# Kernel tuning notes

Hardware: AMD Instinct MI355X
Metric: run time of the kernel (lower is better)

## Reference

```python
import jax, jax.numpy as jnp
import numpy as np

B, S, H = 2, 2048, 1024
E, I = 8, 4096
TOP_K = 2
W_SCALE = 0.02


def setup_inputs() -> dict:
    key = jax.random.key(0)
    k1, k2, k3, k4, k5 = jax.random.split(key, 5)
    return {
        "hidden_states": jax.random.normal(k1, (B, S, H), dtype=jnp.float32),
        "gate_w": jax.random.normal(k2, (H, E), dtype=jnp.float32) * W_SCALE,
        "w1s": jax.random.normal(k3, (E, H, I), dtype=jnp.float32) * W_SCALE,
        "w2s": jax.random.normal(k4, (E, I, H), dtype=jnp.float32) * W_SCALE,
        "w3s": jax.random.normal(k5, (E, H, I), dtype=jnp.float32) * W_SCALE,
    }


def reference(hidden_states, gate_w, w1s, w2s, w3s):
    b, s, h = hidden_states.shape
    x = hidden_states.reshape(-1, h)                      # [T, H]
    # Router: softmax in fp32, top-k, renormalize (matches torch F.softmax(dtype=float) + topk)
    logits = x @ gate_w                                   # [T, E]
    probs = jax.nn.softmax(logits.astype(jnp.float32), axis=-1)
    rw, sel = jax.lax.top_k(probs, TOP_K)                 # [T, K], [T, K]
    rw = rw / jnp.sum(rw, axis=-1, keepdims=True)
    # Per-token combine weight for each expert: [T, E]
    comb = jnp.sum(jax.nn.one_hot(sel, E, dtype=x.dtype) * rw[..., None].astype(x.dtype), axis=1)
    # Expert SwiGLU MLPs; loop over small fixed expert count (same math as grouped GEMM + scatter)
    out = jnp.zeros_like(x)
    for e in range(E):
        inter = jax.nn.silu(x @ w1s[e]) * (x @ w3s[e])    # [T, I]
        out = out + comb[:, e:e + 1] * (inter @ w2s[e])   # [T, H]
    return out.reshape(b, s, h)
```

## Files before the change

kernel.cpp:

```cpp
#include <hip/hip_runtime.h>

#define T_TOK 4096
#define H_DIM 1024
#define I_DIM 4096
#define NE 8
#define INTER_ROWS 9216

typedef _Float16 f16;
typedef _Float16 f16x8 __attribute__((ext_vector_type(8)));
typedef _Float16 f16x4 __attribute__((ext_vector_type(4)));
typedef float f32x4 __attribute__((ext_vector_type(4)));

#define GLOBAL_AS __attribute__((address_space(1)))
#define LDS_AS __attribute__((address_space(3)))

__device__ __forceinline__ void gload_lds16(const void* g, void* l) {
  __builtin_amdgcn_global_load_lds((GLOBAL_AS const unsigned int*)g,
                                   (LDS_AS unsigned int*)l, 16, 0, 0);
}

__global__ void cast_x_kernel(const float* __restrict__ x, f16* __restrict__ xh) {
  int i = blockIdx.x * 256 + threadIdx.x;
  float4 v = reinterpret_cast<const float4*>(x)[i];
  f16x4 o = {(f16)v.x, (f16)v.y, (f16)v.z, (f16)v.w};
  reinterpret_cast<f16x4*>(xh)[i] = o;
}

__global__ __launch_bounds__(256) void transpose_cast_kernel(
    const float* __restrict__ w, f16* __restrict__ wt, int R, int C) {
  __shared__ float tile[64][65];
  const int z = blockIdx.z;
  const float* in = w + (size_t)z * R * C;
  f16* out = wt + (size_t)z * R * C;
  const int c0 = blockIdx.x * 64, r0 = blockIdx.y * 64;
  const int tr = threadIdx.x >> 4;
  const int tc = (threadIdx.x & 15) * 4;
#pragma unroll
  for (int i = 0; i < 4; ++i) {
    int r = tr + i * 16;
    float4 v = *reinterpret_cast<const float4*>(&in[(size_t)(r0 + r) * C + c0 + tc]);
    tile[r][tc] = v.x; tile[r][tc + 1] = v.y; tile[r][tc + 2] = v.z; tile[r][tc + 3] = v.w;
  }
  __syncthreads();
#pragma unroll
  for (int i = 0; i < 4; ++i) {
    int oc = tr + i * 16;
    f16x4 h;
#pragma unroll
    for (int j = 0; j < 4; ++j) h[j] = (f16)tile[tc + j][oc];
    *reinterpret_cast<f16x4*>(&out[(size_t)(c0 + oc) * R + r0 + tc]) = h;
  }
}

__global__ void router_kernel(const float* __restrict__ x, const float* __restrict__ gw,
                              int* __restrict__ counts, int* __restrict__ lists,
                              float* __restrict__ wgts) {
  const int t = blockIdx.x;
  const int l = threadIdx.x;
  const float* xr = x + (size_t)t * H_DIM;
  float acc[NE];
#pragma unroll
  for (int e = 0; e < NE; ++e) acc[e] = 0.f;
  for (int k = l; k < H_DIM; k += 64) {
    float xv = xr[k];
#pragma unroll
    for (int e = 0; e < NE; ++e) acc[e] += xv * gw[k * NE + e];
  }
#pragma unroll
  for (int e = 0; e < NE; ++e) {
    float v = acc[e];
#pragma unroll
    for (int off = 32; off > 0; off >>= 1) v += __shfl_xor(v, off);
    acc[e] = v;
  }
  if (l == 0) {
    int i1 = 0;
#pragma unroll
    for (int e = 1; e < NE; ++e)
      if (acc[e] > acc[i1]) i1 = e;
    int i2 = (i1 == 0) ? 1 : 0;
#pragma unroll
    for (int e = 0; e < NE; ++e)
      if (e != i1 && acc[e] > acc[i2]) i2 = e;
    float wA = 1.f / (1.f + __expf(acc[i2] - acc[i1]));
    float wB = 1.f - wA;
    int p1 = atomicAdd(&counts[i1], 1);
    lists[i1 * T_TOK + p1] = t;
    wgts[i1 * T_TOK + p1] = wA;
    int p2 = atomicAdd(&counts[i2], 1);
    lists[i2 * T_TOK + p2] = t;
    wgts[i2 * T_TOK + p2] = wB;
  }
}

__global__ void prefix_kernel(const int* __restrict__ counts, int* __restrict__ bases) {
  if (threadIdx.x == 0) {
    int s = 0;
#pragma unroll
    for (int e = 0; e < NE; ++e) {
      bases[e] = s;
      s += (counts[e] + 127) & ~127;
    }
  }
}

__global__ __launch_bounds__(256, 2) void gemm_a_kernel(
    const f16* __restrict__ xh, const f16* __restrict__ w1t, const f16* __restrict__ w3t,
    const int* __restrict__ counts, const int* __restrict__ bases,
    const int* __restrict__ lists, f16* __restrict__ inter) {
  const int z = blockIdx.z;
  const int cnt = counts[z];
  const int r0 = blockIdx.y * 128;
  if (r0 >= cnt) return;
  const int base = bases[z];
  const int c0 = blockIdx.x * 128;
  const int tid = threadIdx.x;
  const int lane = tid & 63;
  const int wid = tid >> 6;
  const int wm = wid >> 1, wn = wid & 1;
  const int lrow = lane & 15, lk = lane >> 4;

  __shared__ __align__(16) f16 As[128 * 64];
  __shared__ __align__(16) f16 B1s[128 * 64];
  __shared__ __align__(16) f16 B3s[128 * 64];

  const int* lst = lists + z * T_TOK;
  const f16* w1 = w1t + (size_t)z * H_DIM * I_DIM;
  const f16* w3 = w3t + (size_t)z * H_DIM * I_DIM;

  const f16* asrc[4];
  const f16* b1src[4];
  const f16* b3src[4];
#pragma unroll
  for (int i = 0; i < 4; ++i) {
    int sf = i * 256 + tid;
    int row = sf >> 3;
    int s = sf & 7;
    int cofs = (s ^ (row & 7)) * 8;
    int tok = lst[r0 + row];
    asrc[i] = xh + (size_t)tok * H_DIM + cofs;
    b1src[i] = w1 + (size_t)(c0 + row) * H_DIM + cofs;
    b3src[i] = w3 + (size_t)(c0 + row) * H_DIM + cofs;
  }

  const f32x4 z4 = {0.f, 0.f, 0.f, 0.f};
  f32x4 acc1[4][4], acc3[4][4];
#pragma unroll
  for (int m = 0; m < 4; ++m)
#pragma unroll
    for (int n = 0; n < 4; ++n) { acc1[m][n] = z4; acc3[m][n] = z4; }

  for (int k0 = 0; k0 < H_DIM; k0 += 64) {
#pragma unroll
    for (int i = 0; i < 4; ++i) {
      int ldst = (i * 256 + wid * 64) * 8;
      gload_lds16(asrc[i] + k0, &As[ldst]);
      gload_lds16(b1src[i] + k0, &B1s[ldst]);
      gload_lds16(b3src[i] + k0, &B3s[ldst]);
    }
    __syncthreads();
#pragma unroll
    for (int kk = 0; kk < 2; ++kk) {
      const int cs = kk * 4 + lk;
      f16x8 af[4], b1f[4], b3f[4];
#pragma unroll
      for (int m = 0; m < 4; ++m) {
        int row = wm * 64 + m * 16 + lrow;
        af[m] = *reinterpret_cast<const f16x8*>(&As[row * 64 + ((cs ^ (row & 7)) * 8)]);
      }
#pragma unroll
      for (int n = 0; n < 4; ++n) {
        int row = wn * 64 + n * 16 + lrow;
        int off = row * 64 + ((cs ^ (row & 7)) * 8);
        b1f[n] = *reinterpret_cast<const f16x8*>(&B1s[off]);
        b3f[n] = *reinterpret_cast<const f16x8*>(&B3s[off]);
      }
#pragma unroll
      for (int m = 0; m < 4; ++m)
#pragma unroll
        for (int n = 0; n < 4; ++n) {
          acc1[m][n] = __builtin_amdgcn_mfma_f32_16x16x32_f16(af[m], b1f[n], acc1[m][n], 0, 0, 0);
          acc3[m][n] = __builtin_amdgcn_mfma_f32_16x16x32_f16(af[m], b3f[n], acc3[m][n], 0, 0, 0);
        }
    }
    __syncthreads();
  }
#pragma unroll
  for (int m = 0; m < 4; ++m)
#pragma unroll
    for (int n = 0; n < 4; ++n)
#pragma unroll
      for (int r = 0; r < 4; ++r) {
        int grow = base + r0 + wm * 64 + m * 16 + lk * 4 + r;
        int gcol = c0 + wn * 64 + n * 16 + lrow;
        float s1 = acc1[m][n][r];
        float s3 = acc3[m][n][r];
        float sv = s1 / (1.f + __expf(-s1));
        inter[(size_t)grow * I_DIM + gcol] = (f16)(sv * s3);
      }
}

__global__ __launch_bounds__(256, 2) void gemm_b_kernel(
    const f16* __restrict__ inter, const f16* __restrict__ w2t,
    const int* __restrict__ counts, const int* __restrict__ bases,
    const int* __restrict__ lists, const float* __restrict__ wgts,
    float* __restrict__ out) {
  const int z = blockIdx.z;
  const int cnt = counts[z];
  const int r0 = blockIdx.y * 128;
  if (r0 >= cnt) return;
  const int base = bases[z];
  const int c0 = blockIdx.x * 128;
  const int tid = threadIdx.x;
  const int lane = tid & 63;
  const int wid = tid >> 6;
  const int wm = wid >> 1, wn = wid & 1;
  const int lrow = lane & 15, lk = lane >> 4;

  __shared__ __align__(16) f16 As[128 * 64];
  __shared__ __align__(16) f16 Bs[128 * 64];

  const int* lst = lists + z * T_TOK;
  const float* wgt = wgts + z * T_TOK;
  const f16* w2 = w2t + (size_t)z * I_DIM * H_DIM;

  const f16* asrc[4];
  const f16* bsrc[4];
#pragma unroll
  for (int i = 0; i < 4; ++i) {
    int sf = i * 256 + tid;
    int row = sf >> 3;
    int s = sf & 7;
    int cofs = (s ^ (row & 7)) * 8;
    asrc[i] = inter + (size_t)(base + r0 + row) * I_DIM + cofs;
    bsrc[i] = w2 + (size_t)(c0 + row) * I_DIM + cofs;
  }

  const f32x4 z4 = {0.f, 0.f, 0.f, 0.f};
  f32x4 acc[4][4];
#pragma unroll
  for (int m = 0; m < 4; ++m)
#pragma unroll
    for (int n = 0; n < 4; ++n) acc[m][n] = z4;

  for (int k0 = 0; k0 < I_DIM; k0 += 64) {
#pragma unroll
    for (int i = 0; i < 4; ++i) {
      int ldst = (i * 256 + wid * 64) * 8;
      gload_lds16(asrc[i] + k0, &As[ldst]);
      gload_lds16(bsrc[i] + k0, &Bs[ldst]);
    }
    __syncthreads();
#pragma unroll
    for (int kk = 0; kk < 2; ++kk) {
      const int cs = kk * 4 + lk;
      f16x8 af[4], bf[4];
#pragma unroll
      for (int m = 0; m < 4; ++m) {
        int row = wm * 64 + m * 16 + lrow;
        af[m] = *reinterpret_cast<const f16x8*>(&As[row * 64 + ((cs ^ (row & 7)) * 8)]);
      }
#pragma unroll
      for (int n = 0; n < 4; ++n) {
        int row = wn * 64 + n * 16 + lrow;
        bf[n] = *reinterpret_cast<const f16x8*>(&Bs[row * 64 + ((cs ^ (row & 7)) * 8)]);
      }
#pragma unroll
      for (int m = 0; m < 4; ++m)
#pragma unroll
        for (int n = 0; n < 4; ++n)
          acc[m][n] = __builtin_amdgcn_mfma_f32_16x16x32_f16(af[m], bf[n], acc[m][n], 0, 0, 0);
    }
    __syncthreads();
  }
#pragma unroll
  for (int m = 0; m < 4; ++m)
#pragma unroll
    for (int r = 0; r < 4; ++r) {
      int ri = r0 + wm * 64 + m * 16 + lk * 4 + r;
      if (ri < cnt) {
        int tok = lst[ri];
        float wg = wgt[ri];
        float* orow = out + (size_t)tok * H_DIM + c0 + wn * 64 + lrow;
#pragma unroll
        for (int n = 0; n < 4; ++n) atomicAdd(&orow[n * 16], wg * acc[m][n][r]);
      }
    }
}

extern "C" void kernel_launch(void* const* d_in, const int* in_sizes, int n_in,
                              void* d_out, int out_size, void* d_ws, size_t ws_size,
                              hipStream_t stream) {
  const float* x = (const float*)d_in[0];
  const float* gw = (const float*)d_in[1];
  const float* w1s = (const float*)d_in[2];
  const float* w2s = (const float*)d_in[3];
  const float* w3s = (const float*)d_in[4];
  float* out = (float*)d_out;

  char* ws = (char*)d_ws;
  f16* xh = (f16*)ws;
  f16* inter = (f16*)(ws + ((size_t)8 << 20));
  f16* w1t = (f16*)(ws + ((size_t)80 << 20));
  f16* w3t = (f16*)(ws + ((size_t)144 << 20));
  f16* w2t = (f16*)(ws + ((size_t)208 << 20));
  char* meta = ws + ((size_t)272 << 20);
  int* counts = (int*)meta;
  int* bases = (int*)(meta + 512);
  int* lists = (int*)(meta + 1024);
  float* wgts = (float*)(meta + 1024 + (size_t)NE * T_TOK * 4);

  hipMemsetAsync(out, 0, (size_t)out_size * sizeof(float), stream);
  hipMemsetAsync(meta, 0, 1024 + (size_t)NE * T_TOK * 8, stream);

  cast_x_kernel<<<dim3((T_TOK * H_DIM) / (4 * 256)), dim3(256), 0, stream>>>(x, xh);
  router_kernel<<<dim3(T_TOK), dim3(64), 0, stream>>>(x, gw, counts, lists, wgts);
  prefix_kernel<<<dim3(1), dim3(64), 0, stream>>>(counts, bases);
  transpose_cast_kernel<<<dim3(I_DIM / 64, H_DIM / 64, NE), dim3(256), 0, stream>>>(
      w1s, w1t, H_DIM, I_DIM);
  transpose_cast_kernel<<<dim3(I_DIM / 64, H_DIM / 64, NE), dim3(256), 0, stream>>>(
      w3s, w3t, H_DIM, I_DIM);
  transpose_cast_kernel<<<dim3(H_DIM / 64, I_DIM / 64, NE), dim3(256), 0, stream>>>(
      w2s, w2t, I_DIM, H_DIM);
  gemm_a_kernel<<<dim3(I_DIM / 128, T_TOK / 128, NE), dim3(256), 0, stream>>>(
      xh, w1t, w3t, counts, bases, lists, inter);
  gemm_b_kernel<<<dim3(H_DIM / 128, T_TOK / 128, NE), dim3(256), 0, stream>>>(
      inter, w2t, counts, bases, lists, wgts, out);
}
```

Measured before the change: 536.6 us.

## Triple-buffer LDS ring with 512-thread GEMM blocks and merge weight transposes

Both expert GEMM kernels now use a three-stage LDS ring buffer, prefetching two K-tiles ahead with explicit vmcnt waits and a single barrier per iteration instead of two syncthreads. Blocks grow to 512 threads (8 waves, each covering 64x32 of the tile), which halves per-wave accumulator registers and allows one block per CU with larger LDS. The three weight transpose/cast launches are merged into one launch over a 24-deep grid. The risks are higher LDS usage limiting occupancy and whether the hand-set vmcnt counts match the number of issued loads.

```diff
diff --git a/kernel.cpp b/kernel.cpp
--- a/kernel.cpp
+++ b/kernel.cpp
@@ -4,7 +4,6 @@
 #define H_DIM 1024
 #define I_DIM 4096
 #define NE 8
-#define INTER_ROWS 9216
 
 typedef _Float16 f16;
 typedef _Float16 f16x8 __attribute__((ext_vector_type(8)));
@@ -18,6 +17,11 @@
   __builtin_amdgcn_global_load_lds((GLOBAL_AS const unsigned int*)g,
                                    (LDS_AS unsigned int*)l, 16, 0, 0);
 }
+
+#define VM6() asm volatile("s_waitcnt vmcnt(6)" ::: "memory")
+#define VM4() asm volatile("s_waitcnt vmcnt(4)" ::: "memory")
+#define VM0() asm volatile("s_waitcnt vmcnt(0)" ::: "memory")
+#define BAR() __builtin_amdgcn_s_barrier()
 
 __global__ void cast_x_kernel(const float* __restrict__ x, f16* __restrict__ xh) {
   int i = blockIdx.x * 256 + threadIdx.x;
@@ -27,12 +31,27 @@
 }
 
 __global__ __launch_bounds__(256) void transpose_cast_kernel(
-    const float* __restrict__ w, f16* __restrict__ wt, int R, int C) {
+    const float* __restrict__ w1s, const float* __restrict__ w3s,
+    const float* __restrict__ w2s, f16* __restrict__ w1t,
+    f16* __restrict__ w3t, f16* __restrict__ w2t) {
   __shared__ float tile[64][65];
   const int z = blockIdx.z;
-  const float* in = w + (size_t)z * R * C;
-  f16* out = wt + (size_t)z * R * C;
-  const int c0 = blockIdx.x * 64, r0 = blockIdx.y * 64;
+  const float* in;
+  f16* out;
+  int R, C, r0, c0;
+  if (z < 16) {
+    int e = z & 7;
+    in = (z < 8 ? w1s : w3s) + (size_t)e * H_DIM * I_DIM;
+    out = (z < 8 ? w1t : w3t) + (size_t)e * H_DIM * I_DIM;
+    R = H_DIM; C = I_DIM;
+    c0 = blockIdx.x * 64; r0 = blockIdx.y * 64;
+  } else {
+    int e = z - 16;
+    in = w2s + (size_t)e * H_DIM * I_DIM;
+    out = w2t + (size_t)e * H_DIM * I_DIM;
+    R = I_DIM; C = H_DIM;
+    r0 = blockIdx.x * 64; c0 = blockIdx.y * 64;
+  }
   const int tr = threadIdx.x >> 4;
   const int tc = (threadIdx.x & 15) * 4;
 #pragma unroll
@@ -104,7 +123,7 @@
   }
 }
 
-__global__ __launch_bounds__(256, 2) void gemm_a_kernel(
+__global__ __launch_bounds__(512, 1) void gemm_a_kernel(
     const f16* __restrict__ xh, const f16* __restrict__ w1t, const f16* __restrict__ w3t,
     const int* __restrict__ counts, const int* __restrict__ bases,
     const int* __restrict__ lists, f16* __restrict__ inter) {
@@ -117,23 +136,19 @@
   const int tid = threadIdx.x;
   const int lane = tid & 63;
   const int wid = tid >> 6;
-  const int wm = wid >> 1, wn = wid & 1;
+  const int wm = wid >> 2, wn = wid & 3;
   const int lrow = lane & 15, lk = lane >> 4;
 
-  __shared__ __align__(16) f16 As[128 * 64];
-  __shared__ __align__(16) f16 B1s[128 * 64];
-  __shared__ __align__(16) f16 B3s[128 * 64];
+  __shared__ __align__(16) f16 ring[3][24576];
 
   const int* lst = lists + z * T_TOK;
   const f16* w1 = w1t + (size_t)z * H_DIM * I_DIM;
   const f16* w3 = w3t + (size_t)z * H_DIM * I_DIM;
 
-  const f16* asrc[4];
-  const f16* b1src[4];
-  const f16* b3src[4];
-#pragma unroll
-  for (int i = 0; i < 4; ++i) {
-    int sf = i * 256 + tid;
+  const f16 *asrc[2], *b1src[2], *b3src[2];
+#pragma unroll
+  for (int i = 0; i < 2; ++i) {
+    int sf = i * 512 + tid;
     int row = sf >> 3;
     int s = sf & 7;
     int cofs = (s ^ (row & 7)) * 8;
@@ -143,64 +158,78 @@
     b3src[i] = w3 + (size_t)(c0 + row) * H_DIM + cofs;
   }
 
+#define STAGE_A(SB, K0)                                              \
+  do {                                                               \
+    _Pragma("unroll") for (int i_ = 0; i_ < 2; ++i_) {               \
+      int dofs = (i_ * 512 + (wid << 6)) * 8;                        \
+      gload_lds16(asrc[i_] + (K0), (SB) + dofs);                     \
+      gload_lds16(b1src[i_] + (K0), (SB) + 8192 + dofs);             \
+      gload_lds16(b3src[i_] + (K0), (SB) + 16384 + dofs);            \
+    }                                                                \
+  } while (0)
+
   const f32x4 z4 = {0.f, 0.f, 0.f, 0.f};
-  f32x4 acc1[4][4], acc3[4][4];
+  f32x4 acc1[4][2], acc3[4][2];
 #pragma unroll
   for (int m = 0; m < 4; ++m)
 #pragma unroll
-    for (int n = 0; n < 4; ++n) { acc1[m][n] = z4; acc3[m][n] = z4; }
-
-  for (int k0 = 0; k0 < H_DIM; k0 += 64) {
-#pragma unroll
-    for (int i = 0; i < 4; ++i) {
-      int ldst = (i * 256 + wid * 64) * 8;
-      gload_lds16(asrc[i] + k0, &As[ldst]);
-      gload_lds16(b1src[i] + k0, &B1s[ldst]);
-      gload_lds16(b3src[i] + k0, &B3s[ldst]);
-    }
-    __syncthreads();
+    for (int n = 0; n < 2; ++n) { acc1[m][n] = z4; acc3[m][n] = z4; }
+
+  f16 *s0 = ring[0], *s1 = ring[1], *s2 = ring[2];
+  const int NT = H_DIM / 64;
+  STAGE_A(s0, 0);
+  STAGE_A(s1, 64);
+  VM6();
+  BAR();
+
+  for (int t = 0; t < NT; ++t) {
+    if (t + 2 < NT) STAGE_A(s2, (t + 2) * 64);
 #pragma unroll
     for (int kk = 0; kk < 2; ++kk) {
       const int cs = kk * 4 + lk;
-      f16x8 af[4], b1f[4], b3f[4];
+      f16x8 af[4], b1f[2], b3f[2];
 #pragma unroll
       for (int m = 0; m < 4; ++m) {
         int row = wm * 64 + m * 16 + lrow;
-        af[m] = *reinterpret_cast<const f16x8*>(&As[row * 64 + ((cs ^ (row & 7)) * 8)]);
-      }
-#pragma unroll
-      for (int n = 0; n < 4; ++n) {
-        int row = wn * 64 + n * 16 + lrow;
+        af[m] = *reinterpret_cast<const f16x8*>(&s0[row * 64 + ((cs ^ (row & 7)) * 8)]);
+      }
+#pragma unroll
+      for (int n = 0; n < 2; ++n) {
+        int row = wn * 32 + n * 16 + lrow;
         int off = row * 64 + ((cs ^ (row & 7)) * 8);
-        b1f[n] = *reinterpret_cast<const f16x8*>(&B1s[off]);
-        b3f[n] = *reinterpret_cast<const f16x8*>(&B3s[off]);
+        b1f[n] = *reinterpret_cast<const f16x8*>(&s0[8192 + off]);
+        b3f[n] = *reinterpret_cast<const f16x8*>(&s0[16384 + off]);
       }
 #pragma unroll
       for (int m = 0; m < 4; ++m)
 #pragma unroll
-        for (int n = 0; n < 4; ++n) {
+        for (int n = 0; n < 2; ++n) {
           acc1[m][n] = __builtin_amdgcn_mfma_f32_16x16x32_f16(af[m], b1f[n], acc1[m][n], 0, 0, 0);
           acc3[m][n] = __builtin_amdgcn_mfma_f32_16x16x32_f16(af[m], b3f[n], acc3[m][n], 0, 0, 0);
         }
     }
-    __syncthreads();
-  }
+    if (t + 2 < NT) VM6(); else VM0();
+    BAR();
+    f16* tmp = s0; s0 = s1; s1 = s2; s2 = tmp;
+  }
+#undef STAGE_A
+
 #pragma unroll
   for (int m = 0; m < 4; ++m)
 #pragma unroll
-    for (int n = 0; n < 4; ++n)
+    for (int n = 0; n < 2; ++n)
 #pragma unroll
       for (int r = 0; r < 4; ++r) {
         int grow = base + r0 + wm * 64 + m * 16 + lk * 4 + r;
-        int gcol = c0 + wn * 64 + n * 16 + lrow;
-        float s1 = acc1[m][n][r];
-        float s3 = acc3[m][n][r];
-        float sv = s1 / (1.f + __expf(-s1));
-        inter[(size_t)grow * I_DIM + gcol] = (f16)(sv * s3);
-      }
-}
-
-__global__ __launch_bounds__(256, 2) void gemm_b_kernel(
+        int gcol = c0 + wn * 32 + n * 16 + lrow;
+        float sv1 = acc1[m][n][r];
+        float sv3 = acc3[m][n][r];
+        float sv = sv1 / (1.f + __expf(-sv1));
+        inter[(size_t)grow * I_DIM + gcol] = (f16)(sv * sv3);
+      }
+}
+
+__global__ __launch_bounds__(512, 1) void gemm_b_kernel(
     const f16* __restrict__ inter, const f16* __restrict__ w2t,
     const int* __restrict__ counts, const int* __restrict__ bases,
     const int* __restrict__ lists, const float* __restrict__ wgts,
@@ -214,21 +243,19 @@
   const int tid = threadIdx.x;
   const int lane = tid & 63;
   const int wid = tid >> 6;
-  const int wm = wid >> 1, wn = wid & 1;
+  const int wm = wid >> 2, wn = wid & 3;
   const int lrow = lane & 15, lk = lane >> 4;
 
-  __shared__ __align__(16) f16 As[128 * 64];
-  __shared__ __align__(16) f16 Bs[128 * 64];
+  __shared__ __align__(16) f16 ring[3][16384];
 
   const int* lst = lists + z * T_TOK;
   const float* wgt = wgts + z * T_TOK;
   const f16* w2 = w2t + (size_t)z * I_DIM * H_DIM;
 
-  const f16* asrc[4];
-  const f16* bsrc[4];
-#pragma unroll
-  for (int i = 0; i < 4; ++i) {
-    int sf = i * 256 + tid;
+  const f16 *asrc[2], *bsrc[2];
+#pragma unroll
+  for (int i = 0; i < 2; ++i) {
+    int sf = i * 512 + tid;
     int row = sf >> 3;
     int s = sf & 7;
     int cofs = (s ^ (row & 7)) * 8;
@@ -236,43 +263,57 @@
     bsrc[i] = w2 + (size_t)(c0 + row) * I_DIM + cofs;
   }
 
+#define STAGE_B(SB, K0)                                              \
+  do {                                                               \
+    _Pragma("unroll") for (int i_ = 0; i_ < 2; ++i_) {               \
+      int dofs = (i_ * 512 + (wid << 6)) * 8;                        \
+      gload_lds16(asrc[i_] + (K0), (SB) + dofs);                     \
+      gload_lds16(bsrc[i_] + (K0), (SB) + 8192 + dofs);              \
+    }                                                                \
+  } while (0)
+
   const f32x4 z4 = {0.f, 0.f, 0.f, 0.f};
-  f32x4 acc[4][4];
+  f32x4 acc[4][2];
 #pragma unroll
   for (int m = 0; m < 4; ++m)
 #pragma unroll
-    for (int n = 0; n < 4; ++n) acc[m][n] = z4;
-
-  for (int k0 = 0; k0 < I_DIM; k0 += 64) {
-#pragma unroll
-    for (int i = 0; i < 4; ++i) {
-      int ldst = (i * 256 + wid * 64) * 8;
-      gload_lds16(asrc[i] + k0, &As[ldst]);
-      gload_lds16(bsrc[i] + k0, &Bs[ldst]);
-    }
-    __syncthreads();
+    for (int n = 0; n < 2; ++n) acc[m][n] = z4;
+
+  f16 *s0 = ring[0], *s1 = ring[1], *s2 = ring[2];
+  const int NT = I_DIM / 64;
+  STAGE_B(s0, 0);
+  STAGE_B(s1, 64);
+  VM4();
+  BAR();
+
+  for (int t = 0; t < NT; ++t) {
+    if (t + 2 < NT) STAGE_B(s2, (t + 2) * 64);
 #pragma unroll
     for (int kk = 0; kk < 2; ++kk) {
       const int cs = kk * 4 + lk;
-      f16x8 af[4], bf[4];
+      f16x8 af[4], bf[2];
 #pragma unroll
       for (int m = 0; m < 4; ++m) {
         int row = wm * 64 + m * 16 + lrow;
-        af[m] = *reinterpret_cast<const f16x8*>(&As[row * 64 + ((cs ^ (row & 7)) * 8)]);
-      }
-#pragma unroll
-      for (int n = 0; n < 4; ++n) {
-        int row = wn * 64 + n * 16 + lrow;
-        bf[n] = *reinterpret_cast<const f16x8*>(&Bs[row * 64 + ((cs ^ (row & 7)) * 8)]);
+        af[m] = *reinterpret_cast<const f16x8*>(&s0[row * 64 + ((cs ^ (row & 7)) * 8)]);
+      }
+#pragma unroll
+      for (int n = 0; n < 2; ++n) {
+        int row = wn * 32 + n * 16 + lrow;
+        bf[n] = *reinterpret_cast<const f16x8*>(&s0[8192 + row * 64 + ((cs ^ (row & 7)) * 8)]);
       }
 #pragma unroll
       for (int m = 0; m < 4; ++m)
 #pragma unroll
-        for (int n = 0; n < 4; ++n)
+        for (int n = 0; n < 2; ++n)
           acc[m][n] = __builtin_amdgcn_mfma_f32_16x16x32_f16(af[m], bf[n], acc[m][n], 0, 0, 0);
     }
-    __syncthreads();
-  }
+    if (t + 2 < NT) VM4(); else VM0();
+    BAR();
+    f16* tmp = s0; s0 = s1; s1 = s2; s2 = tmp;
+  }
+#undef STAGE_B
+
 #pragma unroll
   for (int m = 0; m < 4; ++m)
 #pragma unroll
@@ -281,9 +322,9 @@
       if (ri < cnt) {
         int tok = lst[ri];
         float wg = wgt[ri];
-        float* orow = out + (size_t)tok * H_DIM + c0 + wn * 64 + lrow;
-#pragma unroll
-        for (int n = 0; n < 4; ++n) atomicAdd(&orow[n * 16], wg * acc[m][n][r]);
+        float* orow = out + (size_t)tok * H_DIM + c0 + wn * 32 + lrow;
+#pragma unroll
+        for (int n = 0; n < 2; ++n) atomicAdd(&orow[n * 16], wg * acc[m][n][r]);
       }
     }
 }
@@ -316,14 +357,10 @@
   cast_x_kernel<<<dim3((T_TOK * H_DIM) / (4 * 256)), dim3(256), 0, stream>>>(x, xh);
   router_kernel<<<dim3(T_TOK), dim3(64), 0, stream>>>(x, gw, counts, lists, wgts);
   prefix_kernel<<<dim3(1), dim3(64), 0, stream>>>(counts, bases);
-  transpose_cast_kernel<<<dim3(I_DIM / 64, H_DIM / 64, NE), dim3(256), 0, stream>>>(
-      w1s, w1t, H_DIM, I_DIM);
-  transpose_cast_kernel<<<dim3(I_DIM / 64, H_DIM / 64, NE), dim3(256), 0, stream>>>(
-      w3s, w3t, H_DIM, I_DIM);
-  transpose_cast_kernel<<<dim3(H_DIM / 64, I_DIM / 64, NE), dim3(256), 0, stream>>>(
-      w2s, w2t, I_DIM, H_DIM);
-  gemm_a_kernel<<<dim3(I_DIM / 128, T_TOK / 128, NE), dim3(256), 0, stream>>>(
+  transpose_cast_kernel<<<dim3(64, 16, 24), dim3(256), 0, stream>>>(
+      w1s, w3s, w2s, w1t, w3t, w2t);
+  gemm_a_kernel<<<dim3(I_DIM / 128, T_TOK / 128, NE), dim3(512), 0, stream>>>(
       xh, w1t, w3t, counts, bases, lists, inter);
-  gemm_b_kernel<<<dim3(H_DIM / 128, T_TOK / 128, NE), dim3(256), 0, stream>>>(
+  gemm_b_kernel<<<dim3(H_DIM / 128, T_TOK / 128, NE), dim3(512), 0, stream>>>(
       inter, w2t, counts, bases, lists, wgts, out);
 }
```

Measured after the change: 557.4 us. 3.9% more time.
